# Kernel optimization log

Hardware: AMD Instinct MI355X
Metric: run time of the kernel (lower is better)

## Reference

```python
import jax, jax.numpy as jnp
import numpy as np

B, T, D = 8, 1024, 1024
KD, VD, H = 1024, 1024, 16  # key_dim_total, value_dim_total, num_heads
NEG = -1e9
EPS = 1e-5


def setup_inputs() -> dict:
    key = jax.random.key(0)
    ks = jax.random.split(key, 8)
    x = jax.random.normal(ks[0], (B, T, D), dtype=jnp.float32)
    x_lens = jax.random.randint(ks[1], (B,), 1, T + 1).astype(jnp.int32)
    ln_gamma = jnp.ones((D,), jnp.float32)
    ln_beta = jnp.zeros((D,), jnp.float32)
    qkv_out = 2 * KD + VD
    w_qkv = jax.random.normal(ks[2], (D, qkv_out), jnp.float32) / np.sqrt(D)
    b_qkv = jax.random.normal(ks[3], (qkv_out,), jnp.float32) * 0.01
    w_out = jax.random.normal(ks[4], (VD, D), jnp.float32) / np.sqrt(VD)
    b_out = jax.random.normal(ks[5], (D,), jnp.float32) * 0.01
    return {"x": x, "x_lens": x_lens, "ln_gamma": ln_gamma, "ln_beta": ln_beta,
            "w_qkv": w_qkv, "b_qkv": b_qkv, "w_out": w_out, "b_out": b_out}


def reference(x, x_lens, ln_gamma, ln_beta, w_qkv, b_qkv, w_out, b_out):
    # LayerNorm over feature dim
    mu = jnp.mean(x, axis=-1, keepdims=True)
    var = jnp.mean(jnp.square(x - mu), axis=-1, keepdims=True)
    xn = (x - mu) * jax.lax.rsqrt(var + EPS) * ln_gamma + ln_beta
    # fused QKV projection
    qkv = xn @ w_qkv + b_qkv  # (B, T, 2*KD+VD)
    q, k, v = qkv[..., :KD], qkv[..., KD:2 * KD], qkv[..., 2 * KD:]
    hd = KD // H
    q = q.reshape(B, T, H, hd).transpose(0, 2, 1, 3)  # (B,H,T,hd)
    k = k.reshape(B, T, H, hd).transpose(0, 2, 1, 3)
    v = v.reshape(B, T, H, VD // H).transpose(0, 2, 1, 3)
    scale = 1.0 / np.sqrt(hd)
    scores = jnp.einsum("bhtd,bhsd->bhts", q, k) * scale  # (B,H,T,T)
    # combined causal + kv-length padding mask (additive in original; boolean here)
    causal = jnp.tril(jnp.ones((T, T), bool))  # (T,T)
    kv_valid = jnp.arange(T)[None, :] < x_lens[:, None]  # (B,T)
    mask = causal[None, None, :, :] & kv_valid[:, None, None, :]
    scores = jnp.where(mask, scores, NEG)
    att = jax.nn.softmax(scores, axis=-1)
    att_out = jnp.einsum("bhts,bhsd->bhtd", att, v)  # (B,H,T,hd_v)
    out = att_out.transpose(0, 2, 1, 3).reshape(B, T, VD)
    out = out @ w_out + b_out
    return out
```

## Files before the change

kernel.cpp:

```cpp
#include <hip/hip_runtime.h>

#define D_MODEL 1024
#define T_SEQ   1024
#define BATCH   8
#define NHEAD   16
#define HDIM    64

typedef float      v4f   __attribute__((ext_vector_type(4)));
typedef _Float16   half8 __attribute__((ext_vector_type(8)));
typedef _Float16   half4h __attribute__((ext_vector_type(4)));
typedef unsigned int ui4 __attribute__((ext_vector_type(4)));

__device__ __forceinline__ void load_lds16(const _Float16* g, _Float16* l) {
  __builtin_amdgcn_global_load_lds(
      (const __attribute__((address_space(1))) unsigned int*)g,
      (__attribute__((address_space(3))) unsigned int*)l, 16, 0, 0);
}

__global__ __launch_bounds__(256) void ln_kernel(const float* __restrict__ x,
                                                 const float* __restrict__ gamma,
                                                 const float* __restrict__ beta,
                                                 _Float16* __restrict__ xn) {
  int row = blockIdx.x;
  int tid = threadIdx.x;
  const float* xr = x + (size_t)row * D_MODEL;
  v4f xv = *(const v4f*)(xr + tid * 4);
  float s  = xv[0] + xv[1] + xv[2] + xv[3];
  float sq = xv[0]*xv[0] + xv[1]*xv[1] + xv[2]*xv[2] + xv[3]*xv[3];
#pragma unroll
  for (int off = 32; off > 0; off >>= 1) {
    s  += __shfl_xor(s, off);
    sq += __shfl_xor(sq, off);
  }
  __shared__ float ps[4], psq[4];
  int wave = tid >> 6;
  if ((tid & 63) == 0) { ps[wave] = s; psq[wave] = sq; }
  __syncthreads();
  float tot  = ps[0] + ps[1] + ps[2] + ps[3];
  float totq = psq[0] + psq[1] + psq[2] + psq[3];
  float mean = tot * (1.0f / D_MODEL);
  float var  = totq * (1.0f / D_MODEL) - mean * mean;
  float rs   = rsqrtf(var + 1e-5f);
  v4f gv = *(const v4f*)(gamma + tid * 4);
  v4f bv = *(const v4f*)(beta + tid * 4);
  half4h o;
#pragma unroll
  for (int i = 0; i < 4; ++i)
    o[i] = (_Float16)((xv[i] - mean) * rs * gv[i] + bv[i]);
  *(half4h*)(xn + (size_t)row * D_MODEL + tid * 4) = o;
}

__global__ __launch_bounds__(256) void fragize_kernel(const float* __restrict__ W,
                                                      _Float16* __restrict__ Bf,
                                                      int N, int K) {
  int g = blockIdx.x * 256 + threadIdx.x;
  int lane = g & 63, tile = g >> 6;
  int ktiles = K >> 5;
  int kt = tile % ktiles, nt = tile / ktiles;
  int n  = nt * 16 + (lane & 15);
  int k0 = kt * 32 + (lane >> 4) * 8;
  half8 o;
#pragma unroll
  for (int j = 0; j < 8; ++j) o[j] = (_Float16)W[(size_t)(k0 + j) * N + n];
  *(half8*)(Bf + (size_t)g * 8) = o;
}

__global__ __launch_bounds__(256) void vtrans_kernel(const _Float16* __restrict__ Vd,
                                                     _Float16* __restrict__ Vt) {
  __shared__ _Float16 tile[64][68];
  int p  = blockIdx.y;
  int t0 = blockIdx.x * 64;
  int tid = threadIdx.x;
  int r = tid >> 3, c = (tid & 7) * 8;
#pragma unroll
  for (int it = 0; it < 2; ++it) {
    int rr = r + it * 32;
    *(ui4*)&tile[rr][c] = *(const ui4*)&Vd[((size_t)p * T_SEQ + t0 + rr) * HDIM + c];
  }
  __syncthreads();
#pragma unroll
  for (int it = 0; it < 2; ++it) {
    int d = r + it * 32;
    half8 o;
#pragma unroll
    for (int j = 0; j < 8; ++j) o[j] = tile[c + j][d];
    *(half8*)&Vt[((size_t)p * HDIM + d) * T_SEQ + t0 + c] = o;
  }
}

template <int MODE>
__global__ __launch_bounds__(256) void gemm_kernel(
    const _Float16* __restrict__ A, const _Float16* __restrict__ Bfrag,
    const float* __restrict__ bias, int M, int N, int K,
    float* __restrict__ outF,
    _Float16* __restrict__ Qd, _Float16* __restrict__ Kd, _Float16* __restrict__ Vd) {
  __shared__ _Float16 As[128 * 32];
  int tid = threadIdx.x;
  int wave = tid >> 6, lane = tid & 63;
  int l15 = lane & 15, quad = lane >> 4;
  int wm = (wave & 1) * 64, wn = (wave >> 1) * 64;
  int m0 = blockIdx.x * 128, n0 = blockIdx.y * 128;
  v4f zero = {0.f, 0.f, 0.f, 0.f};
  v4f acc[4][4];
#pragma unroll
  for (int i = 0; i < 4; ++i)
#pragma unroll
    for (int j = 0; j < 4; ++j) acc[i][j] = zero;

  int ar0 = tid >> 2;
  int akc = (tid & 3) * 8;
  const _Float16* Ap = A + (size_t)(m0 + ar0) * K + akc;
  _Float16* AsW = As + wave * 512;
  const int ktiles = K >> 5;
  const _Float16* Bp = Bfrag + (size_t)((n0 + wn) >> 4) * ktiles * 512 + lane * 8;

  for (int kt = 0; kt < ktiles; ++kt) {
    half8 bf[4];
#pragma unroll
    for (int ni = 0; ni < 4; ++ni)
      bf[ni] = *(const half8*)(Bp + ((size_t)ni * ktiles + kt) * 512);
    __syncthreads();
    load_lds16(Ap + kt * 32,                  AsW);
    load_lds16(Ap + kt * 32 + (size_t)64 * K, AsW + 2048);
    __syncthreads();
    half8 af[4];
#pragma unroll
    for (int i = 0; i < 4; ++i)
      af[i] = *(const half8*)&As[(wm + i * 16 + l15) * 32 + quad * 8];
#pragma unroll
    for (int mi = 0; mi < 4; ++mi)
#pragma unroll
      for (int ni = 0; ni < 4; ++ni)
        acc[mi][ni] = __builtin_amdgcn_mfma_f32_16x16x32_f16(af[mi], bf[ni], acc[mi][ni], 0, 0, 0);
  }
  float bv[4];
#pragma unroll
  for (int ni = 0; ni < 4; ++ni) bv[ni] = bias[n0 + wn + ni * 16 + l15];
#pragma unroll
  for (int mi = 0; mi < 4; ++mi) {
#pragma unroll
    for (int ni = 0; ni < 4; ++ni) {
      int n = n0 + wn + ni * 16 + l15;
#pragma unroll
      for (int r = 0; r < 4; ++r) {
        int m = m0 + wm + mi * 16 + quad * 4 + r;
        float v = acc[mi][ni][r] + bv[ni];
        if (MODE == 1) {
          outF[(size_t)m * N + n] = v;
        } else {
          int b = m >> 10, t = m & 1023;
          int h = (n >> 6) & 15, d = n & 63;
          size_t idx = ((size_t)(b * NHEAD + h) * T_SEQ + t) * HDIM + d;
          if (n < 1024)        Qd[idx] = (_Float16)(v * 0.18033688f);
          else if (n < 2048)   Kd[idx] = (_Float16)v;
          else                 Vd[idx] = (_Float16)v;
        }
      }
    }
  }
}

__global__ __launch_bounds__(512) void attn_kernel(const _Float16* __restrict__ Kq,
                                                   const _Float16* __restrict__ Kk,
                                                   const _Float16* __restrict__ Vt,
                                                   const int* __restrict__ x_lens,
                                                   _Float16* __restrict__ att) {
  __shared__ _Float16 Ks[2][64 * 32];
  __shared__ _Float16 Vs[2][64 * 32];
  __shared__ _Float16 Pb[8][16 * 72];
  int blk = blockIdx.x;
  int qt = blk >> 7;
  int bh = blk & 127;
  int h  = bh & 15;
  int b  = bh >> 4;
  int t0 = qt * 128;
  int len = x_lens[b];
  int tid = threadIdx.x;
  int wave = tid >> 6, lane = tid & 63;
  int l15 = lane & 15, quad = lane >> 4;
  size_t plane = (size_t)(b * NHEAD + h) * (T_SEQ * HDIM);
  int qrow = t0 + wave * 16;
  const _Float16* Qp = Kq + plane + (size_t)(qrow + l15) * HDIM + quad * 8;
  half8 qf0 = *(const half8*)Qp;
  half8 qf1 = *(const half8*)(Qp + 32);
  v4f zero = {0.f, 0.f, 0.f, 0.f};
  float m_i[4], l_i[4];
  v4f Ov[4];
#pragma unroll
  for (int r = 0; r < 4; ++r) { m_i[r] = -1e30f; l_i[r] = 0.f; }
#pragma unroll
  for (int nt = 0; nt < 4; ++nt) Ov[nt] = zero;

  int jmaxb = min(t0 + 127, len - 1);
  int ntile = (jmaxb >> 6) + 1;
  int wjmax = min(qrow + 15, len - 1);

  int u0 = wave * 2;
  const _Float16* src0;
  const _Float16* src1;
  _Float16* dst0;
  _Float16* dst1;
  {
    int u = u0;
    int q = u & 3, hf = (u >> 2) & 1;
    if (u < 8) {
      src0 = Kk + plane + (size_t)(q * 16 + (lane >> 2)) * HDIM + hf * 32 + (lane & 3) * 8;
      dst0 = &Ks[hf][0] + q * 512;
    } else {
      src0 = Vt + plane + (size_t)(q * 16 + (lane >> 2)) * T_SEQ + hf * 32 + (lane & 3) * 8;
      dst0 = &Vs[hf][0] + q * 512;
    }
    u = u0 + 1;
    q = u & 3; hf = (u >> 2) & 1;
    if (u < 8) {
      src1 = Kk + plane + (size_t)(q * 16 + (lane >> 2)) * HDIM + hf * 32 + (lane & 3) * 8;
      dst1 = &Ks[hf][0] + q * 512;
    } else {
      src1 = Vt + plane + (size_t)(q * 16 + (lane >> 2)) * T_SEQ + hf * 32 + (lane & 3) * 8;
      dst1 = &Vs[hf][0] + q * 512;
    }
  }
  int stride0 = (u0     < 8) ? (64 * HDIM) : 64;
  int stride1 = (u0 + 1 < 8) ? (64 * HDIM) : 64;

  for (int jt = 0; jt < ntile; ++jt) {
    int j0 = jt * 64;
    __syncthreads();
    load_lds16(src0, dst0);
    load_lds16(src1, dst1);
    src0 += stride0;
    src1 += stride1;
    __syncthreads();
    if (j0 <= wjmax) {
      v4f s[4];
#pragma unroll
      for (int nt = 0; nt < 4; ++nt) {
        s[nt] = zero;
        half8 k0 = *(const half8*)&Ks[0][(nt * 16 + l15) * 32 + quad * 8];
        half8 k1 = *(const half8*)&Ks[1][(nt * 16 + l15) * 32 + quad * 8];
        s[nt] = __builtin_amdgcn_mfma_f32_16x16x32_f16(qf0, k0, s[nt], 0, 0, 0);
        s[nt] = __builtin_amdgcn_mfma_f32_16x16x32_f16(qf1, k1, s[nt], 0, 0, 0);
      }
      float rmax[4] = {-1e30f, -1e30f, -1e30f, -1e30f};
      bool full = (j0 + 63 <= qrow) && (j0 + 63 < len);
      if (full) {
#pragma unroll
        for (int nt = 0; nt < 4; ++nt)
#pragma unroll
          for (int r = 0; r < 4; ++r)
            rmax[r] = fmaxf(rmax[r], s[nt][r]);
      } else {
#pragma unroll
        for (int nt = 0; nt < 4; ++nt) {
          int col = j0 + nt * 16 + l15;
#pragma unroll
          for (int r = 0; r < 4; ++r) {
            int trow = qrow + quad * 4 + r;
            float v = (col <= trow && col < len) ? s[nt][r] : -1e30f;
            s[nt][r] = v;
            rmax[r] = fmaxf(rmax[r], v);
          }
        }
      }
#pragma unroll
      for (int off = 1; off < 16; off <<= 1)
#pragma unroll
        for (int r = 0; r < 4; ++r)
          rmax[r] = fmaxf(rmax[r], __shfl_xor(rmax[r], off));
      float alpha[4], rsum[4];
#pragma unroll
      for (int r = 0; r < 4; ++r) {
        float mn = fmaxf(m_i[r], rmax[r]);
        alpha[r] = exp2f(m_i[r] - mn);
        m_i[r] = mn;
        rsum[r] = 0.f;
      }
#pragma unroll
      for (int nt = 0; nt < 4; ++nt)
#pragma unroll
        for (int r = 0; r < 4; ++r) {
          float p = exp2f(s[nt][r] - m_i[r]);
          s[nt][r] = p;
          rsum[r] += p;
        }
#pragma unroll
      for (int off = 1; off < 16; off <<= 1)
#pragma unroll
        for (int r = 0; r < 4; ++r)
          rsum[r] += __shfl_xor(rsum[r], off);
#pragma unroll
      for (int r = 0; r < 4; ++r) l_i[r] = l_i[r] * alpha[r] + rsum[r];
#pragma unroll
      for (int nt = 0; nt < 4; ++nt)
#pragma unroll
        for (int r = 0; r < 4; ++r) Ov[nt][r] *= alpha[r];
#pragma unroll
      for (int nt = 0; nt < 4; ++nt)
#pragma unroll
        for (int r = 0; r < 4; ++r)
          Pb[wave][(quad * 4 + r) * 72 + nt * 16 + l15] = (_Float16)s[nt][r];
      asm volatile("s_waitcnt lgkmcnt(0)" ::: "memory");
      half8 p0 = *(const half8*)&Pb[wave][l15 * 72 + quad * 8];
      half8 p1 = *(const half8*)&Pb[wave][l15 * 72 + quad * 8 + 32];
#pragma unroll
      for (int nt = 0; nt < 4; ++nt) {
        half8 v0 = *(const half8*)&Vs[0][(nt * 16 + l15) * 32 + quad * 8];
        half8 v1 = *(const half8*)&Vs[1][(nt * 16 + l15) * 32 + quad * 8];
        Ov[nt] = __builtin_amdgcn_mfma_f32_16x16x32_f16(p0, v0, Ov[nt], 0, 0, 0);
        Ov[nt] = __builtin_amdgcn_mfma_f32_16x16x32_f16(p1, v1, Ov[nt], 0, 0, 0);
      }
    }
  }
  float inv[4];
#pragma unroll
  for (int r = 0; r < 4; ++r) inv[r] = 1.0f / l_i[r];
#pragma unroll
  for (int nt = 0; nt < 4; ++nt)
#pragma unroll
    for (int r = 0; r < 4; ++r) {
      int trow = qrow + quad * 4 + r;
      att[((size_t)(b * T_SEQ) + trow) * D_MODEL + h * HDIM + nt * 16 + l15] =
          (_Float16)(Ov[nt][r] * inv[r]);
    }
}

extern "C" void kernel_launch(void* const* d_in, const int* in_sizes, int n_in,
                              void* d_out, int out_size, void* d_ws, size_t ws_size,
                              hipStream_t stream) {
  const float* x        = (const float*)d_in[0];
  const int*   x_lens   = (const int*)d_in[1];
  const float* ln_gamma = (const float*)d_in[2];
  const float* ln_beta  = (const float*)d_in[3];
  const float* w_qkv    = (const float*)d_in[4];
  const float* b_qkv    = (const float*)d_in[5];
  const float* w_out    = (const float*)d_in[6];
  const float* b_out    = (const float*)d_in[7];
  float* out = (float*)d_out;

  char* w = (char*)d_ws;
  _Float16* xn    = (_Float16*)w; w += (size_t)8192 * 1024 * 2;
  _Float16* BfQKV = (_Float16*)w; w += (size_t)3072 * 1024 * 2;
  _Float16* BfOut = (_Float16*)w; w += (size_t)1024 * 1024 * 2;
  _Float16* Qd    = (_Float16*)w; w += (size_t)8192 * 1024 * 2;
  _Float16* Kd    = (_Float16*)w; w += (size_t)8192 * 1024 * 2;
  _Float16* Vd    = (_Float16*)w; w += (size_t)8192 * 1024 * 2;
  _Float16* att   = (_Float16*)w; w += (size_t)8192 * 1024 * 2;
  _Float16* Vt    = xn;

  fragize_kernel<<<(3072 * 1024 / 8) / 256, 256, 0, stream>>>(w_qkv, BfQKV, 3072, 1024);
  fragize_kernel<<<(1024 * 1024 / 8) / 256, 256, 0, stream>>>(w_out, BfOut, 1024, 1024);
  ln_kernel<<<8192, 256, 0, stream>>>(x, ln_gamma, ln_beta, xn);
  gemm_kernel<0><<<dim3(8192 / 128, 3072 / 128), 256, 0, stream>>>(
      xn, BfQKV, b_qkv, 8192, 3072, 1024, nullptr, Qd, Kd, Vd);
  vtrans_kernel<<<dim3(16, 128), 256, 0, stream>>>(Vd, Vt);
  attn_kernel<<<1024, 512, 0, stream>>>(Qd, Kd, Vt, x_lens, att);
  gemm_kernel<1><<<dim3(8192 / 128, 1024 / 128), 256, 0, stream>>>(
      att, BfOut, b_out, 8192, 1024, 1024, out, nullptr, nullptr, nullptr);
}
```

Before: 282.9 us.

## Transpose attention score layout and halve query tile per block

The attention kernel now handles 64 query rows per block with 4 waves, launching twice as many blocks. QK^T and PV MFMAs are computed with swapped operands so each lane holds one query row, reducing softmax max/sum reductions to two cross-quad shuffles. Output is staged through LDS and written with vectorized 16-byte stores. Smaller tiles improve causal load balance but reduce K/V reuse per block load.

```diff
diff --git a/kernel.cpp b/kernel.cpp
--- a/kernel.cpp
+++ b/kernel.cpp
@@ -160,76 +160,66 @@
   }
 }
 
-__global__ __launch_bounds__(512) void attn_kernel(const _Float16* __restrict__ Kq,
+__global__ __launch_bounds__(256) void attn_kernel(const _Float16* __restrict__ Qg,
                                                    const _Float16* __restrict__ Kk,
                                                    const _Float16* __restrict__ Vt,
                                                    const int* __restrict__ x_lens,
                                                    _Float16* __restrict__ att) {
   __shared__ _Float16 Ks[2][64 * 32];
   __shared__ _Float16 Vs[2][64 * 32];
-  __shared__ _Float16 Pb[8][16 * 72];
+  __shared__ _Float16 Pb[4][16 * 72];
   int blk = blockIdx.x;
   int qt = blk >> 7;
   int bh = blk & 127;
   int h  = bh & 15;
   int b  = bh >> 4;
-  int t0 = qt * 128;
+  int t0 = qt * 64;
   int len = x_lens[b];
   int tid = threadIdx.x;
   int wave = tid >> 6, lane = tid & 63;
   int l15 = lane & 15, quad = lane >> 4;
   size_t plane = (size_t)(b * NHEAD + h) * (T_SEQ * HDIM);
   int qrow = t0 + wave * 16;
-  const _Float16* Qp = Kq + plane + (size_t)(qrow + l15) * HDIM + quad * 8;
+  int qabs = qrow + l15;
+  const _Float16* Qp = Qg + plane + (size_t)qabs * HDIM + quad * 8;
   half8 qf0 = *(const half8*)Qp;
   half8 qf1 = *(const half8*)(Qp + 32);
   v4f zero = {0.f, 0.f, 0.f, 0.f};
-  float m_i[4], l_i[4];
+  float m_i = -1e30f, l_i = 0.f;
   v4f Ov[4];
 #pragma unroll
-  for (int r = 0; r < 4; ++r) { m_i[r] = -1e30f; l_i[r] = 0.f; }
-#pragma unroll
   for (int nt = 0; nt < 4; ++nt) Ov[nt] = zero;
 
-  int jmaxb = min(t0 + 127, len - 1);
+  int jmaxb = min(t0 + 63, len - 1);
   int ntile = (jmaxb >> 6) + 1;
   int wjmax = min(qrow + 15, len - 1);
 
-  int u0 = wave * 2;
-  const _Float16* src0;
-  const _Float16* src1;
-  _Float16* dst0;
-  _Float16* dst1;
-  {
-    int u = u0;
+  const _Float16* src[4];
+  _Float16* dst[4];
+  int strd[4];
+#pragma unroll
+  for (int i = 0; i < 4; ++i) {
+    int u = wave * 4 + i;
     int q = u & 3, hf = (u >> 2) & 1;
     if (u < 8) {
-      src0 = Kk + plane + (size_t)(q * 16 + (lane >> 2)) * HDIM + hf * 32 + (lane & 3) * 8;
-      dst0 = &Ks[hf][0] + q * 512;
+      src[i] = Kk + plane + (size_t)(q * 16 + (lane >> 2)) * HDIM + hf * 32 + (lane & 3) * 8;
+      dst[i] = &Ks[hf][0] + q * 512;
+      strd[i] = 64 * HDIM;
     } else {
-      src0 = Vt + plane + (size_t)(q * 16 + (lane >> 2)) * T_SEQ + hf * 32 + (lane & 3) * 8;
-      dst0 = &Vs[hf][0] + q * 512;
+      src[i] = Vt + plane + (size_t)(q * 16 + (lane >> 2)) * T_SEQ + hf * 32 + (lane & 3) * 8;
+      dst[i] = &Vs[hf][0] + q * 512;
+      strd[i] = 64;
     }
-    u = u0 + 1;
-    q = u & 3; hf = (u >> 2) & 1;
-    if (u < 8) {
-      src1 = Kk + plane + (size_t)(q * 16 + (lane >> 2)) * HDIM + hf * 32 + (lane & 3) * 8;
-      dst1 = &Ks[hf][0] + q * 512;
-    } else {
-      src1 = Vt + plane + (size_t)(q * 16 + (lane >> 2)) * T_SEQ + hf * 32 + (lane & 3) * 8;
-      dst1 = &Vs[hf][0] + q * 512;
-    }
-  }
-  int stride0 = (u0     < 8) ? (64 * HDIM) : 64;
-  int stride1 = (u0 + 1 < 8) ? (64 * HDIM) : 64;
+  }
 
   for (int jt = 0; jt < ntile; ++jt) {
     int j0 = jt * 64;
     __syncthreads();
-    load_lds16(src0, dst0);
-    load_lds16(src1, dst1);
-    src0 += stride0;
-    src1 += stride1;
+#pragma unroll
+    for (int i = 0; i < 4; ++i) {
+      load_lds16(src[i], dst[i]);
+      src[i] += strd[i];
+    }
     __syncthreads();
     if (j0 <= wjmax) {
       v4f s[4];
@@ -238,90 +228,82 @@
         s[nt] = zero;
         half8 k0 = *(const half8*)&Ks[0][(nt * 16 + l15) * 32 + quad * 8];
         half8 k1 = *(const half8*)&Ks[1][(nt * 16 + l15) * 32 + quad * 8];
-        s[nt] = __builtin_amdgcn_mfma_f32_16x16x32_f16(qf0, k0, s[nt], 0, 0, 0);
-        s[nt] = __builtin_amdgcn_mfma_f32_16x16x32_f16(qf1, k1, s[nt], 0, 0, 0);
-      }
-      float rmax[4] = {-1e30f, -1e30f, -1e30f, -1e30f};
+        s[nt] = __builtin_amdgcn_mfma_f32_16x16x32_f16(k0, qf0, s[nt], 0, 0, 0);
+        s[nt] = __builtin_amdgcn_mfma_f32_16x16x32_f16(k1, qf1, s[nt], 0, 0, 0);
+      }
+      float mnew = m_i;
       bool full = (j0 + 63 <= qrow) && (j0 + 63 < len);
       if (full) {
 #pragma unroll
         for (int nt = 0; nt < 4; ++nt)
 #pragma unroll
           for (int r = 0; r < 4; ++r)
-            rmax[r] = fmaxf(rmax[r], s[nt][r]);
+            mnew = fmaxf(mnew, s[nt][r]);
       } else {
 #pragma unroll
         for (int nt = 0; nt < 4; ++nt) {
-          int col = j0 + nt * 16 + l15;
 #pragma unroll
           for (int r = 0; r < 4; ++r) {
-            int trow = qrow + quad * 4 + r;
-            float v = (col <= trow && col < len) ? s[nt][r] : -1e30f;
+            int key = j0 + nt * 16 + quad * 4 + r;
+            float v = (key <= qabs && key < len) ? s[nt][r] : -1e30f;
             s[nt][r] = v;
-            rmax[r] = fmaxf(rmax[r], v);
+            mnew = fmaxf(mnew, v);
           }
         }
       }
-#pragma unroll
-      for (int off = 1; off < 16; off <<= 1)
-#pragma unroll
-        for (int r = 0; r < 4; ++r)
-          rmax[r] = fmaxf(rmax[r], __shfl_xor(rmax[r], off));
-      float alpha[4], rsum[4];
-#pragma unroll
-      for (int r = 0; r < 4; ++r) {
-        float mn = fmaxf(m_i[r], rmax[r]);
-        alpha[r] = exp2f(m_i[r] - mn);
-        m_i[r] = mn;
-        rsum[r] = 0.f;
-      }
+      mnew = fmaxf(mnew, __shfl_xor(mnew, 16));
+      mnew = fmaxf(mnew, __shfl_xor(mnew, 32));
+      float alpha = exp2f(m_i - mnew);
+      m_i = mnew;
+      float rsum = 0.f;
 #pragma unroll
       for (int nt = 0; nt < 4; ++nt)
 #pragma unroll
         for (int r = 0; r < 4; ++r) {
-          float p = exp2f(s[nt][r] - m_i[r]);
+          float p = exp2f(s[nt][r] - mnew);
           s[nt][r] = p;
-          rsum[r] += p;
+          rsum += p;
         }
-#pragma unroll
-      for (int off = 1; off < 16; off <<= 1)
-#pragma unroll
-        for (int r = 0; r < 4; ++r)
-          rsum[r] += __shfl_xor(rsum[r], off);
-#pragma unroll
-      for (int r = 0; r < 4; ++r) l_i[r] = l_i[r] * alpha[r] + rsum[r];
+      rsum += __shfl_xor(rsum, 16);
+      rsum += __shfl_xor(rsum, 32);
+      l_i = l_i * alpha + rsum;
 #pragma unroll
       for (int nt = 0; nt < 4; ++nt)
 #pragma unroll
-        for (int r = 0; r < 4; ++r) Ov[nt][r] *= alpha[r];
-#pragma unroll
-      for (int nt = 0; nt < 4; ++nt)
-#pragma unroll
-        for (int r = 0; r < 4; ++r)
-          Pb[wave][(quad * 4 + r) * 72 + nt * 16 + l15] = (_Float16)s[nt][r];
+        for (int r = 0; r < 4; ++r) Ov[nt][r] *= alpha;
+#pragma unroll
+      for (int nt = 0; nt < 4; ++nt) {
+        half4h pk;
+#pragma unroll
+        for (int r = 0; r < 4; ++r) pk[r] = (_Float16)s[nt][r];
+        *(half4h*)&Pb[wave][l15 * 72 + nt * 16 + quad * 4] = pk;
+      }
       asm volatile("s_waitcnt lgkmcnt(0)" ::: "memory");
-      half8 p0 = *(const half8*)&Pb[wave][l15 * 72 + quad * 8];
-      half8 p1 = *(const half8*)&Pb[wave][l15 * 72 + quad * 8 + 32];
+      half8 pf0 = *(const half8*)&Pb[wave][l15 * 72 + quad * 8];
+      half8 pf1 = *(const half8*)&Pb[wave][l15 * 72 + 32 + quad * 8];
 #pragma unroll
       for (int nt = 0; nt < 4; ++nt) {
         half8 v0 = *(const half8*)&Vs[0][(nt * 16 + l15) * 32 + quad * 8];
         half8 v1 = *(const half8*)&Vs[1][(nt * 16 + l15) * 32 + quad * 8];
-        Ov[nt] = __builtin_amdgcn_mfma_f32_16x16x32_f16(p0, v0, Ov[nt], 0, 0, 0);
-        Ov[nt] = __builtin_amdgcn_mfma_f32_16x16x32_f16(p1, v1, Ov[nt], 0, 0, 0);
+        Ov[nt] = __builtin_amdgcn_mfma_f32_16x16x32_f16(v0, pf0, Ov[nt], 0, 0, 0);
+        Ov[nt] = __builtin_amdgcn_mfma_f32_16x16x32_f16(v1, pf1, Ov[nt], 0, 0, 0);
       }
     }
   }
-  float inv[4];
-#pragma unroll
-  for (int r = 0; r < 4; ++r) inv[r] = 1.0f / l_i[r];
-#pragma unroll
-  for (int nt = 0; nt < 4; ++nt)
-#pragma unroll
-    for (int r = 0; r < 4; ++r) {
-      int trow = qrow + quad * 4 + r;
-      att[((size_t)(b * T_SEQ) + trow) * D_MODEL + h * HDIM + nt * 16 + l15] =
-          (_Float16)(Ov[nt][r] * inv[r]);
-    }
+  float inv = 1.0f / l_i;
+#pragma unroll
+  for (int nt = 0; nt < 4; ++nt) {
+    half4h ok;
+#pragma unroll
+    for (int r = 0; r < 4; ++r) ok[r] = (_Float16)(Ov[nt][r] * inv);
+    *(half4h*)&Pb[wave][l15 * 72 + nt * 16 + quad * 4] = ok;
+  }
+  asm volatile("s_waitcnt lgkmcnt(0)" ::: "memory");
+  int r0 = lane >> 3, c0 = (lane & 7) * 8;
+  half8 o0 = *(const half8*)&Pb[wave][r0 * 72 + c0];
+  half8 o1 = *(const half8*)&Pb[wave][(r0 + 8) * 72 + c0];
+  *(half8*)&att[((size_t)(b * T_SEQ) + qrow + r0) * D_MODEL + h * HDIM + c0] = o0;
+  *(half8*)&att[((size_t)(b * T_SEQ) + qrow + r0 + 8) * D_MODEL + h * HDIM + c0] = o1;
 }
 
 extern "C" void kernel_launch(void* const* d_in, const int* in_sizes, int n_in,
@@ -353,7 +335,7 @@
   gemm_kernel<0><<<dim3(8192 / 128, 3072 / 128), 256, 0, stream>>>(
       xn, BfQKV, b_qkv, 8192, 3072, 1024, nullptr, Qd, Kd, Vd);
   vtrans_kernel<<<dim3(16, 128), 256, 0, stream>>>(Vd, Vt);
-  attn_kernel<<<1024, 512, 0, stream>>>(Qd, Kd, Vt, x_lens, att);
+  attn_kernel<<<2048, 256, 0, stream>>>(Qd, Kd, Vt, x_lens, att);
   gemm_kernel<1><<<dim3(8192 / 128, 1024 / 128), 256, 0, stream>>>(
       att, BfOut, b_out, 8192, 1024, 1024, out, nullptr, nullptr, nullptr);
 }
```

Result: faster. 264.0 us (-6.7%).
